# Optimization experiments

Hardware: AMD Instinct MI355X
Metric: run time of the kernel (lower is better)

## Reference

```python
import jax, jax.numpy as jnp
import numpy as np

B, N = 2, 1024
DIM = 1024
DQK = 128
NUM_KEYS = 256
NUM_MEM = NUM_KEYS * NUM_KEYS
TOPK = 32
RANK = 2
HEADS = 2
DV = 512
KCONV = 5
MARGIN = 0.15
AUX_W = 0.1
MEM_LR = 10.0
RMS_EPS = 1.1920929e-07  # torch.finfo(float32).eps (RMSNorm eps=None default)
LN_EPS = 1e-5


def setup_inputs() -> dict:
    key = jax.random.key(0)
    ks = jax.random.split(key, 6)
    return {
        "tokens": jax.random.normal(ks[0], (B, N, DIM), jnp.float32),
        "rms_w": jnp.ones((DIM,), jnp.float32),
        "conv_w": jax.random.normal(ks[1], (DIM, 1, KCONV), jnp.float32) * 0.1,
        "conv_b": jnp.zeros((DIM,), jnp.float32),
        "wq": jax.random.normal(ks[2], (DQK, DIM), jnp.float32) * 0.02,
        "qln_w": jnp.ones((DQK,), jnp.float32),
        "keys": jax.random.normal(ks[3], (2, RANK, NUM_KEYS, DQK), jnp.float32) * 0.01,
        "core": jax.random.normal(ks[4], (HEADS, RANK, RANK), jnp.float32) * 0.01,
        "memories": jax.random.normal(ks[5], (NUM_MEM, DV), jnp.float32) * 0.01,
    }


def _forward(tokens, rms_w, conv_w, conv_b, wq, qln_w, keys, core, memories):
    # prenorm RMSNorm
    x = tokens * jax.lax.rsqrt(jnp.mean(tokens * tokens, -1, keepdims=True) + RMS_EPS) * rms_w
    # SVD of core; rank-1 merge vectors (first left/right singular vectors)
    u, s, vh = jnp.linalg.svd(core, full_matrices=False)
    u_vec = u[..., :, 0]   # (H, R)
    t_vec = vh[..., 0, :]  # (H, R)  == v[..., :, 0]
    aux = jnp.sum(jnp.mean(jnp.square(jax.nn.relu(s[:, 1:] - MARGIN)), -1)) * AUX_W
    # causal depthwise conv (left-pad KCONV-1)
    xc = jnp.swapaxes(x, 1, 2)  # (B, D, N)
    xc = jax.lax.conv_general_dilated(
        xc, conv_w, (1,), [(KCONV - 1, 0)],
        feature_group_count=DIM, dimension_numbers=('NCH', 'OIH', 'NCH'))
    x = jnp.swapaxes(xc + conv_b[None, :, None], 1, 2)
    # queries + LayerNorm (no bias). NOTE: original applies key_ln but then uses
    # the raw self.keys in the einsum, so key normalization is a no-op; replicated.
    q = x @ wq.T
    mu = jnp.mean(q, -1, keepdims=True)
    var = jnp.mean(jnp.square(q - mu), -1, keepdims=True)
    q = (q - mu) * jax.lax.rsqrt(var + LN_EPS) * qln_w
    # product-key scores: (2, B, N, M, R)
    sc = jnp.einsum('bnd,crmd->cbnmr', q, keys)
    row_sc, col_sc = sc[0], sc[1]  # (B, N, M, R)
    m_row = jnp.einsum('bnmr,hr->hbnm', row_sc, u_vec)
    m_col = jnp.einsum('bnmr,hr->hbnm', col_sc, t_vec)
    _, top_row = jax.lax.top_k(m_row, TOPK)  # (H, B, N, K)
    _, top_col = jax.lax.top_k(m_col, TOPK)
    # candidate flat memory indices: outer sum -> (H, B, N, K*K)
    idx = (top_row * NUM_KEYS)[..., :, None] + top_col[..., None, :]
    idx = idx.reshape(HEADS, B, N, TOPK * TOPK)
    # gather per-rank scores at the top row/col keys
    rs = jnp.broadcast_to(row_sc[None], (HEADS,) + row_sc.shape)
    cs = jnp.broadcast_to(col_sc[None], (HEADS,) + col_sc.shape)
    ri = jnp.broadcast_to(top_row[..., None], top_row.shape + (RANK,))
    ci = jnp.broadcast_to(top_col[..., None], top_col.shape + (RANK,))
    f_row = jnp.take_along_axis(rs, ri, axis=3)  # (H, B, N, K, R)
    f_col = jnp.take_along_axis(cs, ci, axis=3)
    # bilinear core combine over ranks -> (H, B, N, K, K)
    scores = jnp.einsum('hbnir,hbnjs,hrs->hbnij', f_row, f_col, core)
    scores = scores.reshape(HEADS, B, N, TOPK * TOPK)
    fs, top_m = jax.lax.top_k(scores, TOPK)
    f_idx = jnp.take_along_axis(idx, top_m, axis=-1)  # (H, B, N, K)
    fs = jax.nn.sigmoid(fs)
    # gather from memory table: (H, B, N, K, DV)
    mem = memories[f_idx]
    # scale_gradient exactly as written: detach(t) - s*t + detach(s*t)  (grad = -s)
    scaled = mem * MEM_LR
    mem = jax.lax.stop_gradient(mem) - scaled + jax.lax.stop_gradient(scaled)
    agg = jnp.einsum('hbnkd,hbnk->hbnd', mem, fs)
    out = jnp.transpose(agg, (1, 2, 0, 3)).reshape(B, N, HEADS * DV)
    # combine_values_to_out is Identity (heads * dim_values == dim)
    return out, aux


def reference(tokens, rms_w, conv_w, conv_b, wq, qln_w, keys, core, memories):
    return _forward(tokens, rms_w, conv_w, conv_b, wq, qln_w, keys, core, memories)
```

## Files before the change

### kernel.cpp

```cpp
#include <hip/hip_runtime.h>
#include <math.h>


#define ROWS 2048

__device__ inline double dsgn(double x, double y) { return (y >= 0.0) ? fabs(x) : -fabs(x); }

__device__ void dlasv2_dev(double f, double g, double h,
                           double& ssmin, double& ssmax,
                           double& snr, double& csr, double& snl, double& csl)
{
  const double EPSD = 2.2204460492503131e-16;
  double ft = f, fa = fabs(f), ht = h, ha = fabs(h);
  int pmax = 1;
  bool swp = (ha > fa);
  if (swp) { pmax = 3; double tp = ft; ft = ht; ht = tp; tp = fa; fa = ha; ha = tp; }
  double gt = g, ga = fabs(gt);
  double clt = 0.0, crt = 0.0, slt = 0.0, srt = 0.0;
  if (ga == 0.0) {
    ssmin = ha; ssmax = fa; clt = 1.0; crt = 1.0; slt = 0.0; srt = 0.0;
  } else {
    bool gasmal = true;
    if (ga > fa) {
      pmax = 2;
      if ((fa / ga) < EPSD) {
        gasmal = false;
        ssmax = ga;
        if (ha > 1.0) ssmin = fa / (ga / ha); else ssmin = (fa / ga) * ha;
        clt = 1.0; slt = ht / gt; srt = 1.0; crt = ft / gt;
      }
    }
    if (gasmal) {
      double dd = fa - ha, l;
      if (dd == fa) l = 1.0; else l = dd / fa;
      double m  = gt / ft;
      double t  = 2.0 - l;
      double mm = m * m, tt = t * t;
      double s  = sqrt(tt + mm);
      double r  = (l == 0.0) ? fabs(m) : sqrt(l * l + mm);
      double a  = 0.5 * (s + r);
      ssmin = ha / a;
      ssmax = fa * a;
      if (mm == 0.0) {
        if (l == 0.0) t = dsgn(2.0, ft) * dsgn(1.0, gt);
        else          t = gt / dsgn(dd, ft) + m / t;
      } else {
        t = (m / (s + t) + m / (r + l)) * (1.0 + a);
      }
      double ll = sqrt(t * t + 4.0);
      crt = 2.0 / ll;
      srt = t / ll;
      clt = (crt + srt * m) / a;
      slt = (ht / ft) * srt / a;
    }
  }
  if (swp) { csl = srt; snl = crt; csr = slt; snr = clt; }
  else     { csl = clt; snl = slt; csr = crt; snr = srt; }
  double tsign = 1.0;
  if (pmax == 1) tsign = dsgn(1.0, csr) * dsgn(1.0, csl) * dsgn(1.0, f);
  if (pmax == 2) tsign = dsgn(1.0, snr) * dsgn(1.0, csl) * dsgn(1.0, g);
  if (pmax == 3) tsign = dsgn(1.0, snr) * dsgn(1.0, snl) * dsgn(1.0, h);
  ssmax = dsgn(ssmax, tsign);
  ssmin = dsgn(ssmin, tsign * dsgn(1.0, f) * dsgn(1.0, h));
}

__global__ void svd_kernel(const float* __restrict__ core, float* __restrict__ misc,
                           float* __restrict__ aux_out)
{
  if (threadIdx.x != 0 || blockIdx.x != 0) return;
  double aux = 0.0;
  for (int hh = 0; hh < 2; hh++) {
    double a = (double)core[hh * 4 + 0];
    double b = (double)core[hh * 4 + 1];
    double c = (double)core[hh * 4 + 2];
    double d = (double)core[hh * 4 + 3];
    double tau = 0.0, v2 = 0.0, d1, e, d2;
    if (c != 0.0) {
      double nrm  = sqrt(a * a + c * c);
      double beta = (a >= 0.0) ? -nrm : nrm;
      tau = (beta - a) / beta;
      v2  = c / (a - beta);
      double wsum = b + v2 * d;
      d1 = beta;
      e  = b - tau * wsum;
      d2 = d - tau * v2 * wsum;
    } else { d1 = a; e = b; d2 = d; }
    double ssmin, ssmax, snr, csr, snl, csl;
    dlasv2_dev(d1, e, d2, ssmin, ssmax, snr, csr, snl, csl);
    double t0 = csl + v2 * snl;
    double u0 = csl - tau * t0;
    double u1 = snl - tau * v2 * t0;
    double sg = (ssmax < 0.0) ? -1.0 : 1.0;
    misc[hh * 2 + 0]     = (float)u0;
    misc[hh * 2 + 1]     = (float)u1;
    misc[4 + hh * 2 + 0] = (float)(sg * csr);
    misc[4 + hh * 2 + 1] = (float)(sg * snr);
    double s2 = fabs(ssmin);
    double rl = s2 - 0.15; if (rl < 0.0) rl = 0.0;
    aux += rl * rl;
  }
  aux_out[0] = (float)(aux * 0.1);
}

__global__ __launch_bounds__(256) void conv_kernel(const float* __restrict__ tokens,
                                                   const float* __restrict__ rms_w,
                                                   const float* __restrict__ conv_w,
                                                   const float* __restrict__ conv_b,
                                                   float* __restrict__ x2)
{
  __shared__ float x_l[12][1024];
  __shared__ float red[12][4];
  __shared__ float inv_s[12];
  const int t    = threadIdx.x;
  const int row0 = blockIdx.x * 8;
  const int n0   = row0 & 1023;
  const int c0   = t * 4;

  float sq[12];
  #pragma unroll
  for (int s = 0; s < 12; s++) {
    float4 v = make_float4(0.f, 0.f, 0.f, 0.f);
    if (n0 - 4 + s >= 0)
      v = *(const float4*)(tokens + (size_t)(row0 - 4 + s) * 1024 + c0);
    *(float4*)&x_l[s][c0] = v;
    sq[s] = v.x * v.x + v.y * v.y + v.z * v.z + v.w * v.w;
  }
  #pragma unroll
  for (int off = 32; off; off >>= 1) {
    #pragma unroll
    for (int s = 0; s < 12; s++) sq[s] += __shfl_down(sq[s], off, 64);
  }
  const int lane = t & 63, wv_id = t >> 6;
  if (lane == 0) {
    #pragma unroll
    for (int s = 0; s < 12; s++) red[s][wv_id] = sq[s];
  }
  __syncthreads();
  if (t < 12)
    inv_s[t] = rsqrtf((red[t][0] + red[t][1] + red[t][2] + red[t][3]) * (1.0f / 1024.0f)
                      + 1.1920929e-07f);
  __syncthreads();
  #pragma unroll
  for (int s = 0; s < 12; s++) {
    float iv = inv_s[s];
    float4 v = *(float4*)&x_l[s][c0];
    v.x *= iv; v.y *= iv; v.z *= iv; v.w *= iv;
    *(float4*)&x_l[s][c0] = v;
  }
  float wv[20];
  const float* cw = conv_w + (size_t)c0 * 5;
  #pragma unroll
  for (int i = 0; i < 5; i++) {
    float4 u = *(const float4*)(cw + i * 4);
    wv[i * 4 + 0] = u.x; wv[i * 4 + 1] = u.y; wv[i * 4 + 2] = u.z; wv[i * 4 + 3] = u.w;
  }
  float4 rw = *(const float4*)(rms_w + c0);
  float4 cb = *(const float4*)(conv_b + c0);
  #pragma unroll
  for (int r = 0; r < 8; r++) {
    float4 acc = make_float4(0.f, 0.f, 0.f, 0.f);
    #pragma unroll
    for (int k = 0; k < 5; k++) {
      float4 x4 = *(const float4*)&x_l[r + k][c0];
      acc.x = fmaf(x4.x, wv[0 * 5 + k], acc.x);
      acc.y = fmaf(x4.y, wv[1 * 5 + k], acc.y);
      acc.z = fmaf(x4.z, wv[2 * 5 + k], acc.z);
      acc.w = fmaf(x4.w, wv[3 * 5 + k], acc.w);
    }
    acc.x = acc.x * rw.x + cb.x;
    acc.y = acc.y * rw.y + cb.y;
    acc.z = acc.z * rw.z + cb.z;
    acc.w = acc.w * rw.w + cb.w;
    *(float4*)(x2 + (size_t)(row0 + r) * 1024 + c0) = acc;
  }
}

__global__ __launch_bounds__(256) void gemm_kernel(const float* __restrict__ A, int lda,
                                                   const float* __restrict__ Bm, int ldb,
                                                   float* __restrict__ C, int ldc,
                                                   int koffy, int coffy, int poffy)
{
  __shared__ __align__(16) float a_lds[32 * 64];
  __shared__ __align__(16) float b_lds[32 * 128];
  const int t  = threadIdx.x;
  const int rb = blockIdx.x * 64;
  const int kb = blockIdx.y * koffy;
  const int cb = blockIdx.y * coffy;
  C += (size_t)blockIdx.y * (size_t)poffy;
  const int tx = t & 31, ty = t >> 5;
  const int c0 = tx * 4, r0 = ty * 8;
  float acc[8][4];
  #pragma unroll
  for (int i = 0; i < 8; i++)
    #pragma unroll
    for (int j = 0; j < 4; j++) acc[i][j] = 0.0f;

  const int ra = t & 63,  kqa = (t >> 6) * 8;
  const int ob = t >> 1,  kqb = (t & 1) * 16;

  for (int kt = 0; kt < 4; kt++) {
    const int k0 = kb + kt * 32;
    {
      const float* ap = A + (size_t)(rb + ra) * lda + k0 + kqa;
      float4 a0 = *(const float4*)(ap);
      float4 a1 = *(const float4*)(ap + 4);
      a_lds[(kqa + 0) * 64 + ra] = a0.x;
      a_lds[(kqa + 1) * 64 + ra] = a0.y;
      a_lds[(kqa + 2) * 64 + ra] = a0.z;
      a_lds[(kqa + 3) * 64 + ra] = a0.w;
      a_lds[(kqa + 4) * 64 + ra] = a1.x;
      a_lds[(kqa + 5) * 64 + ra] = a1.y;
      a_lds[(kqa + 6) * 64 + ra] = a1.z;
      a_lds[(kqa + 7) * 64 + ra] = a1.w;
    }
    {
      const float* bp = Bm + (size_t)(cb + ob) * ldb + k0 + kqb;
      float4 b0 = *(const float4*)(bp);
      float4 b1 = *(const float4*)(bp + 4);
      float4 b2 = *(const float4*)(bp + 8);
      float4 b3 = *(const float4*)(bp + 12);
      b_lds[(kqb +  0) * 128 + ob] = b0.x;
      b_lds[(kqb +  1) * 128 + ob] = b0.y;
      b_lds[(kqb +  2) * 128 + ob] = b0.z;
      b_lds[(kqb +  3) * 128 + ob] = b0.w;
      b_lds[(kqb +  4) * 128 + ob] = b1.x;
      b_lds[(kqb +  5) * 128 + ob] = b1.y;
      b_lds[(kqb +  6) * 128 + ob] = b1.z;
      b_lds[(kqb +  7) * 128 + ob] = b1.w;
      b_lds[(kqb +  8) * 128 + ob] = b2.x;
      b_lds[(kqb +  9) * 128 + ob] = b2.y;
      b_lds[(kqb + 10) * 128 + ob] = b2.z;
      b_lds[(kqb + 11) * 128 + ob] = b2.w;
      b_lds[(kqb + 12) * 128 + ob] = b3.x;
      b_lds[(kqb + 13) * 128 + ob] = b3.y;
      b_lds[(kqb + 14) * 128 + ob] = b3.z;
      b_lds[(kqb + 15) * 128 + ob] = b3.w;
    }
    __syncthreads();
    #pragma unroll
    for (int k = 0; k < 32; k++) {
      float4 av0 = *(const float4*)(a_lds + k * 64 + r0);
      float4 av1 = *(const float4*)(a_lds + k * 64 + r0 + 4);
      float4 bv  = *(const float4*)(b_lds + k * 128 + c0);
      float ar[8] = {av0.x, av0.y, av0.z, av0.w, av1.x, av1.y, av1.z, av1.w};
      float br[4] = {bv.x, bv.y, bv.z, bv.w};
      #pragma unroll
      for (int i = 0; i < 8; i++)
        #pragma unroll
        for (int j = 0; j < 4; j++)
          acc[i][j] = fmaf(ar[i], br[j], acc[i][j]);
    }
    __syncthreads();
  }
  #pragma unroll
  for (int i = 0; i < 8; i++) {
    float4 o4; o4.x = acc[i][0]; o4.y = acc[i][1]; o4.z = acc[i][2]; o4.w = acc[i][3];
    *(float4*)(C + (size_t)(rb + r0 + i) * ldc + cb + c0) = o4;
  }
}

__global__ __launch_bounds__(128) void ln_kernel(const float* __restrict__ qpart,
                                                 const float* __restrict__ qln_w,
                                                 float* __restrict__ q)
{
  const int row = blockIdx.x, o = threadIdx.x;
  float v = 0.0f;
  #pragma unroll
  for (int g = 0; g < 8; g++) v += qpart[(size_t)g * (ROWS * 128) + (size_t)row * 128 + o];
  __shared__ float red[2];
  float s = v;
  for (int off = 32; off; off >>= 1) s += __shfl_down(s, off, 64);
  if ((o & 63) == 0) red[o >> 6] = s;
  __syncthreads();
  float mu  = (red[0] + red[1]) * (1.0f / 128.0f);
  float dv  = v - mu;
  float s2  = dv * dv;
  for (int off = 32; off; off >>= 1) s2 += __shfl_down(s2, off, 64);
  __syncthreads();
  if ((o & 63) == 0) red[o >> 6] = s2;
  __syncthreads();
  float var = (red[0] + red[1]) * (1.0f / 128.0f);
  q[(size_t)row * 128 + o] = dv * rsqrtf(var + 1e-5f) * qln_w[o];
}

__device__ inline unsigned f2ord(float f) {
  unsigned u = __float_as_uint(f);
  return (u & 0x80000000u) ? ~u : (u | 0x80000000u);
}
__device__ inline int lpc(unsigned long long m) {
  return __builtin_amdgcn_mbcnt_hi((unsigned)(m >> 32),
         __builtin_amdgcn_mbcnt_lo((unsigned)m, 0));
}

__global__ __launch_bounds__(256) void select_kernel(const float* __restrict__ sc,
                                                     const float* __restrict__ misc,
                                                     const float* __restrict__ core,
                                                     int*   __restrict__ sel_i,
                                                     float* __restrict__ sel_w)
{
  __shared__ __align__(16) float s_pl[1024];
  __shared__ int   tkbuf[4][32];
  __shared__ float mvals[4][32];
  __shared__ int   mcand[4][32];

  const int row = blockIdx.x;
  const int tid = threadIdx.x;
  ((float4*)s_pl)[tid] = ((const float4*)(sc + (size_t)row * 1024))[tid];
  __syncthreads();

  const int w = tid >> 6, lane = tid & 63;

  {
    const int h = w >> 1, side = w & 1;
    const float v0 = misc[side * 4 + h * 2 + 0];
    const float v1 = misc[side * 4 + h * 2 + 1];
    const float* p0 = s_pl + side * 512;
    const float* p1 = p0 + 256;
    const int mb = lane * 4;
    float4 a4 = *(const float4*)(p0 + mb);
    float4 b4 = *(const float4*)(p1 + mb);
    unsigned kk[4];
    kk[0] = f2ord(a4.x * v0 + b4.x * v1);
    kk[1] = f2ord(a4.y * v0 + b4.y * v1);
    kk[2] = f2ord(a4.z * v0 + b4.z * v1);
    kk[3] = f2ord(a4.w * v0 + b4.w * v1);
    unsigned tau = 0u;
    #pragma unroll
    for (int b = 31; b >= 0; --b) {
      unsigned cand = tau | (1u << b);
      int cnt = 0;
      #pragma unroll
      for (int i = 0; i < 4; i++) cnt += __popcll(__ballot(kk[i] >= cand));
      if (cnt >= 32) tau = cand;
    }
    unsigned long long bG[4], bE[4];
    int cntG = 0, sbG = 0, sbE = 0;
    #pragma unroll
    for (int i = 0; i < 4; i++) {
      bG[i] = __ballot(kk[i] > tau);
      bE[i] = __ballot(kk[i] == tau);
      cntG += __popcll(bG[i]);
      sbG  += lpc(bG[i]);
      sbE  += lpc(bE[i]);
    }
    const int need = 32 - cntG;
    int runG = 0, runE = 0;
    #pragma unroll
    for (int i = 0; i < 4; i++) {
      if (kk[i] > tau)       { tkbuf[w][sbG + runG] = mb + i; runG++; }
      else if (kk[i] == tau) {
        int r = sbE + runE;
        if (r < need) tkbuf[w][cntG + r] = mb + i;
        runE++;
      }
    }
  }
  __syncthreads();

  {
    const int h = w >> 1, half = w & 1;
    const float c00 = core[h * 4 + 0], c01 = core[h * 4 + 1];
    const float c10 = core[h * 4 + 2], c11 = core[h * 4 + 3];
    const int i_glob = half * 16 + (lane >> 2);
    const int ri = tkbuf[h * 2 + 0][i_glob];
    const float fr0 = s_pl[ri], fr1 = s_pl[256 + ri];
    const float a0 = fr0 * c00 + fr1 * c10;
    const float a1 = fr0 * c01 + fr1 * c11;
    const int j0 = (lane & 3) * 8;
    float sv[8];
    unsigned kk[8];
    #pragma unroll
    for (int t2 = 0; t2 < 8; t2++) {
      int cj = tkbuf[h * 2 + 1][j0 + t2];
      sv[t2] = a0 * s_pl[512 + cj] + a1 * s_pl[768 + cj];
      kk[t2] = f2ord(sv[t2]);
    }
    unsigned tau = 0u;
    #pragma unroll
    for (int b = 31; b >= 0; --b) {
      unsigned cand = tau | (1u << b);
      int cnt = 0;
      #pragma unroll
      for (int i = 0; i < 8; i++) cnt += __popcll(__ballot(kk[i] >= cand));
      if (cnt >= 32) tau = cand;
    }
    unsigned long long bG[8], bE[8];
    int cntG = 0, sbG = 0, sbE = 0;
    #pragma unroll
    for (int i = 0; i < 8; i++) {
      bG[i] = __ballot(kk[i] > tau);
      bE[i] = __ballot(kk[i] == tau);
      cntG += __popcll(bG[i]);
      sbG  += lpc(bG[i]);
      sbE  += lpc(bE[i]);
    }
    const int need = 32 - cntG;
    int runG = 0, runE = 0;
    #pragma unroll
    for (int i = 0; i < 8; i++) {
      int c = i_glob * 32 + j0 + i;
      if (kk[i] > tau) {
        mvals[w][sbG + runG] = sv[i]; mcand[w][sbG + runG] = c; runG++;
      } else if (kk[i] == tau) {
        int r = sbE + runE;
        if (r < need) { mvals[w][cntG + r] = sv[i]; mcand[w][cntG + r] = c; }
        runE++;
      }
    }
  }
  __syncthreads();

  if (w < 2) {
    const int h = w;
    const int half2 = lane >> 5, k = lane & 31;
    const float v = mvals[h * 2 + half2][k];
    const int   c = mcand[h * 2 + half2][k];
    int cnt = 0;
    #pragma unroll 8
    for (int j = 0; j < 64; j++) {
      float u = mvals[h * 2 + (j >> 5)][j & 31];
      int  uc = mcand[h * 2 + (j >> 5)][j & 31];
      cnt += (u > v || (u == v && uc < c)) ? 1 : 0;
    }
    if (cnt < 32) {
      int ii = c >> 5, jj = c & 31;
      sel_i[(size_t)row * 64 + h * 32 + cnt] = tkbuf[h * 2][ii] * 256 + tkbuf[h * 2 + 1][jj];
      sel_w[(size_t)row * 64 + h * 32 + cnt] = 1.0f / (1.0f + expf(-v));
    }
  }
}

__global__ __launch_bounds__(256) void gather_kernel(const int*   __restrict__ sel_i,
                                                     const float* __restrict__ sel_w,
                                                     const float* __restrict__ memories,
                                                     float* __restrict__ out)
{
  __shared__ int   s_idx[64];
  __shared__ float s_w[64];
  const int row = blockIdx.x;
  const int tid = threadIdx.x;
  if (tid < 64) {
    s_idx[tid] = sel_i[(size_t)row * 64 + tid];
    s_w[tid]   = sel_w[(size_t)row * 64 + tid];
  }
  __syncthreads();
  const int h2 = tid >> 7;
  const int d4 = tid & 127;
  const float* mb = memories + d4 * 4;
  float ax = 0.f, ay = 0.f, az = 0.f, aw = 0.f;
  #pragma unroll
  for (int b = 0; b < 4; b++) {
    int   mi[8]; float wg[8]; float4 v[8];
    #pragma unroll
    for (int i = 0; i < 8; i++) {
      mi[i] = s_idx[h2 * 32 + b * 8 + i];
      wg[i] = s_w[h2 * 32 + b * 8 + i];
    }
    #pragma unroll
    for (int i = 0; i < 8; i++)
      v[i] = *(const float4*)(mb + (size_t)mi[i] * 512);
    #pragma unroll
    for (int i = 0; i < 8; i++) {
      ax = fmaf(wg[i], v[i].x, ax);
      ay = fmaf(wg[i], v[i].y, ay);
      az = fmaf(wg[i], v[i].z, az);
      aw = fmaf(wg[i], v[i].w, aw);
    }
  }
  float4 o4; o4.x = ax; o4.y = ay; o4.z = az; o4.w = aw;
  ((float4*)out)[(size_t)row * 256 + tid] = o4;
}

extern "C" void kernel_launch(void* const* d_in, const int* in_sizes, int n_in,
                              void* d_out, int out_size, void* d_ws, size_t ws_size,
                              hipStream_t stream) {
  const float* tokens = (const float*)d_in[0];
  const float* rms_w  = (const float*)d_in[1];
  const float* conv_w = (const float*)d_in[2];
  const float* conv_b = (const float*)d_in[3];
  const float* wq     = (const float*)d_in[4];
  const float* qln_w  = (const float*)d_in[5];
  const float* keys   = (const float*)d_in[6];
  const float* core   = (const float*)d_in[7];
  const float* mems   = (const float*)d_in[8];
  float* out = (float*)d_out;
  float* ws  = (float*)d_ws;

  float* misc   = ws;
  float* x2     = ws + 4096;
  float* qpart  = x2 + 2097152;
  float* q      = qpart + 2097152;
  float* sc     = x2;
  int*   sel_i  = (int*)qpart;
  float* sel_w  = qpart + 131072;

  svd_kernel   <<<1, 64, 0, stream>>>(core, misc, out + 2097152);
  conv_kernel  <<<ROWS / 8, 256, 0, stream>>>(tokens, rms_w, conv_w, conv_b, x2);
  gemm_kernel  <<<dim3(32, 8), 256, 0, stream>>>(x2, 1024, wq, 1024,
                                                 qpart, 128, 128, 0, ROWS * 128);
  ln_kernel    <<<ROWS, 128, 0, stream>>>(qpart, qln_w, q);
  gemm_kernel  <<<dim3(32, 8), 256, 0, stream>>>(q, 128, keys, 128,
                                                 sc, 1024, 0, 128, 0);
  select_kernel<<<ROWS, 256, 0, stream>>>(sc, misc, core, sel_i, sel_w);
  gather_kernel<<<ROWS, 256, 0, stream>>>(sel_i, sel_w, mems, out);
}
```

Baseline: 286.2 us.

## Fuse SVD into conv, LayerNorm into second GEMM, and select with gather

Cuts the launch count from seven to four. The SVD runs on one thread at the end of the conv kernel, and the split-K reduction plus LayerNorm moves into the prologue of the keys GEMM, which keeps the normalized q tile in LDS. Selection and the memory gather are merged so indices and weights stay in shared memory, and the gather loads are double-buffered. The trade-offs are extra serial work on the first conv block, the split-K partials being re-reduced by each of the 8 column blocks, and higher register pressure in the tail kernel.

Result: faster. 277.6 us (-3.0%).

```diff
diff --git a/kernel.cpp b/kernel.cpp
--- a/kernel.cpp
+++ b/kernel.cpp
@@ -64,10 +64,9 @@
   ssmin = dsgn(ssmin, tsign * dsgn(1.0, f) * dsgn(1.0, h));
 }
 
-__global__ void svd_kernel(const float* __restrict__ core, float* __restrict__ misc,
-                           float* __restrict__ aux_out)
+__device__ void do_svd(const float* __restrict__ core, float* __restrict__ misc,
+                       float* __restrict__ aux_out)
 {
-  if (threadIdx.x != 0 || blockIdx.x != 0) return;
   double aux = 0.0;
   for (int hh = 0; hh < 2; hh++) {
     double a = (double)core[hh * 4 + 0];
@@ -106,6 +105,9 @@
                                                    const float* __restrict__ rms_w,
                                                    const float* __restrict__ conv_w,
                                                    const float* __restrict__ conv_b,
+                                                   const float* __restrict__ core,
+                                                   float* __restrict__ misc,
+                                                   float* __restrict__ aux_out,
                                                    float* __restrict__ x2)
 {
   __shared__ float x_l[12][1024];
@@ -173,6 +175,7 @@
     acc.w = acc.w * rw.w + cb.w;
     *(float4*)(x2 + (size_t)(row0 + r) * 1024 + c0) = acc;
   }
+  if (blockIdx.x == 0 && t == 0) do_svd(core, misc, aux_out);
 }
 
 __global__ __launch_bounds__(256) void gemm_kernel(const float* __restrict__ A, int lda,
@@ -259,28 +262,106 @@
   }
 }
 
-__global__ __launch_bounds__(128) void ln_kernel(const float* __restrict__ qpart,
-                                                 const float* __restrict__ qln_w,
-                                                 float* __restrict__ q)
+__global__ __launch_bounds__(256) void gemm2ln_kernel(const float* __restrict__ qpart,
+                                                      const float* __restrict__ qln_w,
+                                                      const float* __restrict__ keys,
+                                                      float* __restrict__ C)
 {
-  const int row = blockIdx.x, o = threadIdx.x;
-  float v = 0.0f;
-  #pragma unroll
-  for (int g = 0; g < 8; g++) v += qpart[(size_t)g * (ROWS * 128) + (size_t)row * 128 + o];
-  __shared__ float red[2];
-  float s = v;
-  for (int off = 32; off; off >>= 1) s += __shfl_down(s, off, 64);
-  if ((o & 63) == 0) red[o >> 6] = s;
-  __syncthreads();
-  float mu  = (red[0] + red[1]) * (1.0f / 128.0f);
-  float dv  = v - mu;
-  float s2  = dv * dv;
-  for (int off = 32; off; off >>= 1) s2 += __shfl_down(s2, off, 64);
-  __syncthreads();
-  if ((o & 63) == 0) red[o >> 6] = s2;
-  __syncthreads();
-  float var = (red[0] + red[1]) * (1.0f / 128.0f);
-  q[(size_t)row * 128 + o] = dv * rsqrtf(var + 1e-5f) * qln_w[o];
+  __shared__ __align__(16) float a_l[128 * 64];
+  __shared__ __align__(16) float b_lds[32 * 128];
+  const int t  = threadIdx.x;
+  const int rb = blockIdx.x * 64;
+  const int cb = blockIdx.y * 128;
+
+  const int l32 = t & 31;
+  const int g32 = t >> 5;
+  float vs[8][4];
+  #pragma unroll
+  for (int j = 0; j < 8; j++) { vs[j][0]=0.f; vs[j][1]=0.f; vs[j][2]=0.f; vs[j][3]=0.f; }
+  #pragma unroll
+  for (int g = 0; g < 8; g++) {
+    const float* pg = qpart + (size_t)g * (ROWS * 128) + (size_t)rb * 128 + l32 * 4;
+    #pragma unroll
+    for (int j = 0; j < 8; j++) {
+      float4 v = *(const float4*)(pg + (g32 + 8 * j) * 128);
+      vs[j][0] += v.x; vs[j][1] += v.y; vs[j][2] += v.z; vs[j][3] += v.w;
+    }
+  }
+  float4 qw = *(const float4*)(qln_w + l32 * 4);
+  #pragma unroll
+  for (int j = 0; j < 8; j++) {
+    float s1 = vs[j][0] + vs[j][1] + vs[j][2] + vs[j][3];
+    #pragma unroll
+    for (int off = 16; off; off >>= 1) s1 += __shfl_xor(s1, off, 32);
+    float mu = s1 * (1.0f / 128.0f);
+    float d0 = vs[j][0] - mu, d1 = vs[j][1] - mu, d2 = vs[j][2] - mu, d3 = vs[j][3] - mu;
+    float s2 = d0 * d0 + d1 * d1 + d2 * d2 + d3 * d3;
+    #pragma unroll
+    for (int off = 16; off; off >>= 1) s2 += __shfl_xor(s2, off, 32);
+    float rstd = rsqrtf(s2 * (1.0f / 128.0f) + 1e-5f);
+    const int row = g32 + 8 * j;
+    a_l[(l32 * 4 + 0) * 64 + row] = d0 * rstd * qw.x;
+    a_l[(l32 * 4 + 1) * 64 + row] = d1 * rstd * qw.y;
+    a_l[(l32 * 4 + 2) * 64 + row] = d2 * rstd * qw.z;
+    a_l[(l32 * 4 + 3) * 64 + row] = d3 * rstd * qw.w;
+  }
+  __syncthreads();
+
+  const int tx = t & 31, ty = t >> 5;
+  const int c0 = tx * 4, r0 = ty * 8;
+  float acc[8][4];
+  #pragma unroll
+  for (int i = 0; i < 8; i++)
+    #pragma unroll
+    for (int j = 0; j < 4; j++) acc[i][j] = 0.0f;
+
+  const int ob = t >> 1, kqb = (t & 1) * 16;
+  for (int kt = 0; kt < 4; kt++) {
+    const int k0 = kt * 32;
+    {
+      const float* bp = keys + (size_t)(cb + ob) * 128 + k0 + kqb;
+      float4 b0 = *(const float4*)(bp);
+      float4 b1 = *(const float4*)(bp + 4);
+      float4 b2 = *(const float4*)(bp + 8);
+      float4 b3 = *(const float4*)(bp + 12);
+      b_lds[(kqb +  0) * 128 + ob] = b0.x;
+      b_lds[(kqb +  1) * 128 + ob] = b0.y;
+      b_lds[(kqb +  2) * 128 + ob] = b0.z;
+      b_lds[(kqb +  3) * 128 + ob] = b0.w;
+      b_lds[(kqb +  4) * 128 + ob] = b1.x;
+      b_lds[(kqb +  5) * 128 + ob] = b1.y;
+      b_lds[(kqb +  6) * 128 + ob] = b1.z;
+      b_lds[(kqb +  7) * 128 + ob] = b1.w;
+      b_lds[(kqb +  8) * 128 + ob] = b2.x;
+      b_lds[(kqb +  9) * 128 + ob] = b2.y;
+      b_lds[(kqb + 10) * 128 + ob] = b2.z;
+      b_lds[(kqb + 11) * 128 + ob] = b2.w;
+      b_lds[(kqb + 12) * 128 + ob] = b3.x;
+      b_lds[(kqb + 13) * 128 + ob] = b3.y;
+      b_lds[(kqb + 14) * 128 + ob] = b3.z;
+      b_lds[(kqb + 15) * 128 + ob] = b3.w;
+    }
+    __syncthreads();
+    #pragma unroll
+    for (int k = 0; k < 32; k++) {
+      float4 av0 = *(const float4*)(a_l + (k0 + k) * 64 + r0);
+      float4 av1 = *(const float4*)(a_l + (k0 + k) * 64 + r0 + 4);
+      float4 bv  = *(const float4*)(b_lds + k * 128 + c0);
+      float ar[8] = {av0.x, av0.y, av0.z, av0.w, av1.x, av1.y, av1.z, av1.w};
+      float br[4] = {bv.x, bv.y, bv.z, bv.w};
+      #pragma unroll
+      for (int i = 0; i < 8; i++)
+        #pragma unroll
+        for (int j = 0; j < 4; j++)
+          acc[i][j] = fmaf(ar[i], br[j], acc[i][j]);
+    }
+    __syncthreads();
+  }
+  #pragma unroll
+  for (int i = 0; i < 8; i++) {
+    float4 o4; o4.x = acc[i][0]; o4.y = acc[i][1]; o4.z = acc[i][2]; o4.w = acc[i][3];
+    *(float4*)(C + (size_t)(rb + r0 + i) * 1024 + cb + c0) = o4;
+  }
 }
 
 __device__ inline unsigned f2ord(float f) {
@@ -292,16 +373,18 @@
          __builtin_amdgcn_mbcnt_lo((unsigned)m, 0));
 }
 
-__global__ __launch_bounds__(256) void select_kernel(const float* __restrict__ sc,
-                                                     const float* __restrict__ misc,
-                                                     const float* __restrict__ core,
-                                                     int*   __restrict__ sel_i,
-                                                     float* __restrict__ sel_w)
+__global__ __launch_bounds__(256) void tail_kernel(const float* __restrict__ sc,
+                                                   const float* __restrict__ misc,
+                                                   const float* __restrict__ core,
+                                                   const float* __restrict__ memories,
+                                                   float* __restrict__ out)
 {
   __shared__ __align__(16) float s_pl[1024];
   __shared__ int   tkbuf[4][32];
   __shared__ float mvals[4][32];
   __shared__ int   mcand[4][32];
+  __shared__ int   s_idx[64];
+  __shared__ float s_w[64];
 
   const int row = blockIdx.x;
   const int tid = threadIdx.x;
@@ -424,48 +507,58 @@
     }
     if (cnt < 32) {
       int ii = c >> 5, jj = c & 31;
-      sel_i[(size_t)row * 64 + h * 32 + cnt] = tkbuf[h * 2][ii] * 256 + tkbuf[h * 2 + 1][jj];
-      sel_w[(size_t)row * 64 + h * 32 + cnt] = 1.0f / (1.0f + expf(-v));
-    }
-  }
-}
-
-__global__ __launch_bounds__(256) void gather_kernel(const int*   __restrict__ sel_i,
-                                                     const float* __restrict__ sel_w,
-                                                     const float* __restrict__ memories,
-                                                     float* __restrict__ out)
-{
-  __shared__ int   s_idx[64];
-  __shared__ float s_w[64];
-  const int row = blockIdx.x;
-  const int tid = threadIdx.x;
-  if (tid < 64) {
-    s_idx[tid] = sel_i[(size_t)row * 64 + tid];
-    s_w[tid]   = sel_w[(size_t)row * 64 + tid];
-  }
-  __syncthreads();
+      s_idx[h * 32 + cnt] = tkbuf[h * 2][ii] * 256 + tkbuf[h * 2 + 1][jj];
+      s_w[h * 32 + cnt]   = 1.0f / (1.0f + expf(-v));
+    }
+  }
+  __syncthreads();
+
   const int h2 = tid >> 7;
   const int d4 = tid & 127;
+  const int base = h2 * 32;
   const float* mb = memories + d4 * 4;
   float ax = 0.f, ay = 0.f, az = 0.f, aw = 0.f;
-  #pragma unroll
-  for (int b = 0; b < 4; b++) {
-    int   mi[8]; float wg[8]; float4 v[8];
-    #pragma unroll
-    for (int i = 0; i < 8; i++) {
-      mi[i] = s_idx[h2 * 32 + b * 8 + i];
-      wg[i] = s_w[h2 * 32 + b * 8 + i];
-    }
-    #pragma unroll
-    for (int i = 0; i < 8; i++)
-      v[i] = *(const float4*)(mb + (size_t)mi[i] * 512);
-    #pragma unroll
-    for (int i = 0; i < 8; i++) {
-      ax = fmaf(wg[i], v[i].x, ax);
-      ay = fmaf(wg[i], v[i].y, ay);
-      az = fmaf(wg[i], v[i].z, az);
-      aw = fmaf(wg[i], v[i].w, aw);
-    }
+  float4 va[8], vb[8];
+  float  wa[8], wb[8];
+  #pragma unroll
+  for (int i = 0; i < 8; i++) {
+    int mi = s_idx[base + i]; wa[i] = s_w[base + i];
+    va[i] = *(const float4*)(mb + (size_t)mi * 512);
+  }
+  #pragma unroll
+  for (int i = 0; i < 8; i++) {
+    int mi = s_idx[base + 8 + i]; wb[i] = s_w[base + 8 + i];
+    vb[i] = *(const float4*)(mb + (size_t)mi * 512);
+  }
+  #pragma unroll
+  for (int i = 0; i < 8; i++) {
+    ax = fmaf(wa[i], va[i].x, ax); ay = fmaf(wa[i], va[i].y, ay);
+    az = fmaf(wa[i], va[i].z, az); aw = fmaf(wa[i], va[i].w, aw);
+  }
+  #pragma unroll
+  for (int i = 0; i < 8; i++) {
+    int mi = s_idx[base + 16 + i]; wa[i] = s_w[base + 16 + i];
+    va[i] = *(const float4*)(mb + (size_t)mi * 512);
+  }
+  #pragma unroll
+  for (int i = 0; i < 8; i++) {
+    ax = fmaf(wb[i], vb[i].x, ax); ay = fmaf(wb[i], vb[i].y, ay);
+    az = fmaf(wb[i], vb[i].z, az); aw = fmaf(wb[i], vb[i].w, aw);
+  }
+  #pragma unroll
+  for (int i = 0; i < 8; i++) {
+    int mi = s_idx[base + 24 + i]; wb[i] = s_w[base + 24 + i];
+    vb[i] = *(const float4*)(mb + (size_t)mi * 512);
+  }
+  #pragma unroll
+  for (int i = 0; i < 8; i++) {
+    ax = fmaf(wa[i], va[i].x, ax); ay = fmaf(wa[i], va[i].y, ay);
+    az = fmaf(wa[i], va[i].z, az); aw = fmaf(wa[i], va[i].w, aw);
+  }
+  #pragma unroll
+  for (int i = 0; i < 8; i++) {
+    ax = fmaf(wb[i], vb[i].x, ax); ay = fmaf(wb[i], vb[i].y, ay);
+    az = fmaf(wb[i], vb[i].z, az); aw = fmaf(wb[i], vb[i].w, aw);
   }
   float4 o4; o4.x = ax; o4.y = ay; o4.z = az; o4.w = aw;
   ((float4*)out)[(size_t)row * 256 + tid] = o4;
@@ -489,18 +582,12 @@
   float* misc   = ws;
   float* x2     = ws + 4096;
   float* qpart  = x2 + 2097152;
-  float* q      = qpart + 2097152;
   float* sc     = x2;
-  int*   sel_i  = (int*)qpart;
-  float* sel_w  = qpart + 131072;
-
-  svd_kernel   <<<1, 64, 0, stream>>>(core, misc, out + 2097152);
-  conv_kernel  <<<ROWS / 8, 256, 0, stream>>>(tokens, rms_w, conv_w, conv_b, x2);
+
+  conv_kernel  <<<ROWS / 8, 256, 0, stream>>>(tokens, rms_w, conv_w, conv_b,
+                                              core, misc, out + 2097152, x2);
   gemm_kernel  <<<dim3(32, 8), 256, 0, stream>>>(x2, 1024, wq, 1024,
                                                  qpart, 128, 128, 0, ROWS * 128);
-  ln_kernel    <<<ROWS, 128, 0, stream>>>(qpart, qln_w, q);
-  gemm_kernel  <<<dim3(32, 8), 256, 0, stream>>>(q, 128, keys, 128,
-                                                 sc, 1024, 0, 128, 0);
-  select_kernel<<<ROWS, 256, 0, stream>>>(sc, misc, core, sel_i, sel_w);
-  gather_kernel<<<ROWS, 256, 0, stream>>>(sel_i, sel_w, mems, out);
-}
+  gemm2ln_kernel<<<dim3(32, 8), 256, 0, stream>>>(qpart, qln_w, keys, sc);
+  tail_kernel  <<<ROWS, 256, 0, stream>>>(sc, misc, core, mems, out);
+}
```
